# Performance work log

Hardware: AMD Instinct MI355X
Metric: run time of the kernel (lower is better)

## Reference

```python
import jax, jax.numpy as jnp
import numpy as np

B, D, E, K, H, C = 8192, 1024, 8, 2, 2048, 512
LN_EPS = 1e-5


def setup_inputs() -> dict:
    key = jax.random.key(0)
    ks = jax.random.split(key, 6)
    s = 0.02
    return {
        "x": jax.random.normal(ks[0], (B, D), dtype=jnp.float32),
        "Wr": jax.random.normal(ks[1], (E, D), dtype=jnp.float32) * s,  # router weight [E,D]
        "br": jnp.zeros((E,), dtype=jnp.float32),
        "gamma": jnp.ones((E, D), dtype=jnp.float32),   # per-expert LayerNorm scale
        "beta": jnp.zeros((E, D), dtype=jnp.float32),   # per-expert LayerNorm shift
        "W1": jax.random.normal(ks[2], (E, H, D), dtype=jnp.float32) * s,
        "b1": jnp.zeros((E, H), dtype=jnp.float32),
        "W2": jax.random.normal(ks[3], (E, C, H), dtype=jnp.float32) * s,
        "b2": jnp.zeros((E, C), dtype=jnp.float32),
    }


def reference(x, Wr, br, gamma, beta, W1, b1, W2, b2):
    # Router + top-k gating (softmax over the k selected logits only)
    router_logits = x @ Wr.T + br                       # [B,E]
    topk_vals, topk_idx = jax.lax.top_k(router_logits, K)  # [B,K]
    topk_w = jax.nn.softmax(topk_vals, axis=-1)         # [B,K]
    # Dense gate [B,E]: gate[b,e] = sum_j topk_w[b,j] * (topk_idx[b,j]==e)
    gate = (jax.nn.one_hot(topk_idx, E, dtype=x.dtype) * topk_w[..., None]).sum(axis=1)

    # LayerNorm statistics are expert-independent; affine is per-expert
    mu = x.mean(axis=-1, keepdims=True)
    var = ((x - mu) ** 2).mean(axis=-1, keepdims=True)
    xn = (x - mu) * jax.lax.rsqrt(var + LN_EPS)          # [B,D]

    out = jnp.zeros((x.shape[0], C), dtype=x.dtype)
    for e in range(E):  # small fixed expert count
        xe = xn * gamma[e] + beta[e]                     # [B,D]
        h = jax.nn.gelu(xe @ W1[e].T + b1[e], approximate=False)  # [B,H]
        y = h @ W2[e].T + b2[e]                          # [B,C]
        out = out + gate[:, e:e + 1] * y
    return out
```

## Files before the change

kernel.cpp:

```cpp
#include <hip/hip_runtime.h>
#include <hip/hip_bf16.h>
#include <math.h>

#define B_TOK 8192
#define DDIM 1024
#define NEXP 8
#define HDIM 2048
#define CDIM 512
#define LN_EPS 1e-5f
#define MAXT256 72
#define MAXROWS (MAXT256 * 256)

typedef __attribute__((ext_vector_type(4))) float f32x4;
typedef __attribute__((ext_vector_type(8))) short bf16x8;

__device__ __forceinline__ unsigned short f2bf(float f) {
  __hip_bfloat16 h = __float2bfloat16(f);
  return *reinterpret_cast<unsigned short*>(&h);
}
__device__ __forceinline__ float bf2f(unsigned short u) {
  unsigned int x = ((unsigned int)u) << 16;
  return *reinterpret_cast<float*>(&x);
}

__device__ __forceinline__ void gload_lds16(const unsigned short* g, unsigned short* l) {
  __builtin_amdgcn_global_load_lds(
      (const __attribute__((address_space(1))) unsigned int*)g,
      (__attribute__((address_space(3))) unsigned int*)l, 16, 0, 0);
}

__global__ __launch_bounds__(256) void router_ln_kernel(
    const float* __restrict__ x, const float* __restrict__ Wr,
    const float* __restrict__ br, int* __restrict__ eidx,
    float* __restrict__ wgt, unsigned short* __restrict__ xn) {
  const int wid = threadIdx.x >> 6;
  const int lane = threadIdx.x & 63;
  const int tok = blockIdx.x * 4 + wid;

  const float4* xr = reinterpret_cast<const float4*>(x + (size_t)tok * DDIM);
  float4 xv[4];
  float sum = 0.f, sumsq = 0.f;
  float dot[NEXP];
#pragma unroll
  for (int e = 0; e < NEXP; ++e) dot[e] = 0.f;

#pragma unroll
  for (int i = 0; i < 4; ++i) {
    const int f = i * 64 + lane;
    float4 v = xr[f];
    xv[i] = v;
    sum += v.x + v.y + v.z + v.w;
    sumsq += v.x * v.x + v.y * v.y + v.z * v.z + v.w * v.w;
#pragma unroll
    for (int e = 0; e < NEXP; ++e) {
      float4 w = reinterpret_cast<const float4*>(Wr + e * DDIM)[f];
      dot[e] += v.x * w.x + v.y * w.y + v.z * w.z + v.w * w.w;
    }
  }
#pragma unroll
  for (int off = 32; off > 0; off >>= 1) {
    sum += __shfl_xor(sum, off);
    sumsq += __shfl_xor(sumsq, off);
#pragma unroll
    for (int e = 0; e < NEXP; ++e) dot[e] += __shfl_xor(dot[e], off);
  }
  const float mu = sum * (1.f / DDIM);
  const float var = sumsq * (1.f / DDIM) - mu * mu;
  const float rs = rsqrtf(var + LN_EPS);

  float lg[NEXP];
#pragma unroll
  for (int e = 0; e < NEXP; ++e) lg[e] = dot[e] + br[e];

  int i1 = 0; float v1 = lg[0];
#pragma unroll
  for (int e = 1; e < NEXP; ++e) { if (lg[e] > v1) { v1 = lg[e]; i1 = e; } }
  int i2 = -1; float v2 = -3.4e38f;
#pragma unroll
  for (int e = 0; e < NEXP; ++e) { if (e != i1 && lg[e] > v2) { v2 = lg[e]; i2 = e; } }

  const float e2 = __expf(v2 - v1);
  const float inv = 1.f / (1.f + e2);
  if (lane == 0) {
    eidx[tok * 2] = i1; eidx[tok * 2 + 1] = i2;
    wgt[tok * 2] = inv; wgt[tok * 2 + 1] = e2 * inv;
  }

  unsigned short* xnr = xn + (size_t)tok * DDIM;
#pragma unroll
  for (int i = 0; i < 4; ++i) {
    const int f = i * 64 + lane;
    float4 v = xv[i];
    ushort4 o;
    o.x = f2bf((v.x - mu) * rs);
    o.y = f2bf((v.y - mu) * rs);
    o.z = f2bf((v.z - mu) * rs);
    o.w = f2bf((v.w - mu) * rs);
    reinterpret_cast<ushort4*>(xnr)[f] = o;
  }
}

__global__ __launch_bounds__(256) void sort_kernel(
    const int* __restrict__ eidx,
    int* __restrict__ tokRow,
    int* __restrict__ slot2row,
    int* __restrict__ tileExp,
    int* __restrict__ nTilesOut) {
  __shared__ int cnt[NEXP], segBase[NEXP], cur[NEXP];
  const int tid = threadIdx.x;
  if (tid < NEXP) { cnt[tid] = 0; cur[tid] = 0; }
  __syncthreads();
  for (int t = tid; t < B_TOK * 2; t += 256)
    atomicAdd(&cnt[eidx[t]], 1);
  __syncthreads();
  if (tid == 0) {
    int c = 0;
    for (int e = 0; e < NEXP; ++e) {
      segBase[e] = c;
      const int nt = (cnt[e] + 255) >> 8;
      for (int t = 0; t < nt; ++t) tileExp[(c >> 8) + t] = e;
      for (int p = c + cnt[e]; p < c + nt * 256; ++p) tokRow[p] = 0;
      c += nt * 256;
    }
    *nTilesOut = c >> 8;
  }
  __syncthreads();
  for (int t = tid; t < B_TOK * 2; t += 256) {
    const int e = eidx[t];
    const int pos = segBase[e] + atomicAdd(&cur[e], 1);
    tokRow[pos] = t >> 1;
    slot2row[t] = pos;
  }
}

__global__ __launch_bounds__(256) void prep_w1_kernel(
    const float* __restrict__ W1, const float* __restrict__ gamma,
    const float* __restrict__ beta, const float* __restrict__ b1,
    unsigned short* __restrict__ W1g, float* __restrict__ c1) {
  const int eh = blockIdx.x;
  const int e = eh >> 11;
  const int tid = threadIdx.x;

  float4 w = reinterpret_cast<const float4*>(W1 + (size_t)eh * DDIM)[tid];
  float4 g = reinterpret_cast<const float4*>(gamma + (size_t)e * DDIM)[tid];
  float4 bt = reinterpret_cast<const float4*>(beta + (size_t)e * DDIM)[tid];

  ushort4 o;
  o.x = f2bf(w.x * g.x); o.y = f2bf(w.y * g.y);
  o.z = f2bf(w.z * g.z); o.w = f2bf(w.w * g.w);
  reinterpret_cast<ushort4*>(W1g + (size_t)eh * DDIM)[tid] = o;

  float p = w.x * bt.x + w.y * bt.y + w.z * bt.z + w.w * bt.w;
#pragma unroll
  for (int off = 32; off > 0; off >>= 1) p += __shfl_xor(p, off);
  __shared__ float red[4];
  const int lane = tid & 63, wv = tid >> 6;
  if (lane == 0) red[wv] = p;
  __syncthreads();
  if (tid == 0) c1[eh] = b1[eh] + red[0] + red[1] + red[2] + red[3];
}

__global__ __launch_bounds__(256) void prep_w2_kernel(
    const float* __restrict__ W2, unsigned short* __restrict__ W2b) {
  const int idx = blockIdx.x * 256 + threadIdx.x;
  float4 w = reinterpret_cast<const float4*>(W2)[idx];
  ushort4 o;
  o.x = f2bf(w.x); o.y = f2bf(w.y); o.z = f2bf(w.z); o.w = f2bf(w.w);
  reinterpret_cast<ushort4*>(W2b)[idx] = o;
}

#define BM 128
#define BN 128
#define BKK 64

__global__ __launch_bounds__(256) void gemm1_gelu_kernel(
    const unsigned short* __restrict__ A,
    const unsigned short* __restrict__ W1g,
    const float* __restrict__ c1,
    const int* __restrict__ tokRow, const int* __restrict__ tileExp,
    const int* __restrict__ nTiles,
    unsigned short* __restrict__ Hout) {
  const int flat = blockIdx.x;
  const int p = flat & 7;
  const int q = flat >> 3;
  const int by = p * 2 + (q / 144);
  const int bx = q % 144;
  if ((bx >> 1) >= *nTiles) return;
  const int e = tileExp[bx >> 1];

  __shared__ unsigned short lA[BM * BKK];
  __shared__ unsigned short lB[BN * BKK];
  const int tid = threadIdx.x;
  const int lane = tid & 63;
  const int wid = tid >> 6;
  const int wr = wid >> 1, wc = wid & 1;
  const int l15 = lane & 15, l4 = lane >> 4;

  const unsigned short* Bbase = W1g + ((size_t)e * HDIM + (size_t)by * BN) * DDIM;

  const int r = tid >> 3;
  const int swz = ((tid & 7) ^ (r & 7)) * 8;
  const int dst = (tid & 7) * 8;
  int aRow[4];
#pragma unroll
  for (int i = 0; i < 4; ++i) aRow[i] = tokRow[bx * BM + i * 32 + r];

  f32x4 acc[4][4];
#pragma unroll
  for (int m = 0; m < 4; ++m)
#pragma unroll
    for (int n = 0; n < 4; ++n)
#pragma unroll
      for (int j = 0; j < 4; ++j) acc[m][n][j] = 0.f;

  for (int k0 = 0; k0 < DDIM; k0 += BKK) {
#pragma unroll
    for (int i = 0; i < 4; ++i)
      gload_lds16(A + (size_t)aRow[i] * DDIM + k0 + swz,
                  &lA[(i * 32 + r) * BKK + dst]);
#pragma unroll
    for (int i = 0; i < 4; ++i)
      gload_lds16(Bbase + (size_t)(i * 32 + r) * DDIM + k0 + swz,
                  &lB[(i * 32 + r) * BKK + dst]);
    __syncthreads();
#pragma unroll
    for (int kk = 0; kk < 2; ++kk) {
      bf16x8 af[4], bfr[4];
      const int slot = (((kk * 4 + l4) ^ (l15 & 7)) * 8);
#pragma unroll
      for (int m = 0; m < 4; ++m)
        af[m] = *reinterpret_cast<const bf16x8*>(
            &lA[(wr * 64 + m * 16 + l15) * BKK + slot]);
#pragma unroll
      for (int n = 0; n < 4; ++n)
        bfr[n] = *reinterpret_cast<const bf16x8*>(
            &lB[(wc * 64 + n * 16 + l15) * BKK + slot]);
#pragma unroll
      for (int m = 0; m < 4; ++m)
#pragma unroll
        for (int n = 0; n < 4; ++n)
          acc[m][n] = __builtin_amdgcn_mfma_f32_16x16x32_bf16(af[m], bfr[n], acc[m][n], 0, 0, 0);
    }
    __syncthreads();
  }

  const int row0 = bx * BM + wr * 64;
  const int col0 = by * BN + wc * 64;
  const float* bias = c1 + e * HDIM;
#pragma unroll
  for (int n = 0; n < 4; ++n) {
    const int col = col0 + n * 16 + l15;
    const float bv = bias[col];
#pragma unroll
    for (int m = 0; m < 4; ++m) {
#pragma unroll
      for (int j = 0; j < 4; ++j) {
        const int row = row0 + m * 16 + l4 * 4 + j;
        const float v = acc[m][n][j] + bv;
        const float gl = 0.5f * v * (1.f + erff(v * 0.70710678118654752f));
        Hout[(size_t)row * HDIM + col] = f2bf(gl);
      }
    }
  }
}

__global__ __launch_bounds__(256) void gemm2_kernel(
    const unsigned short* __restrict__ Hbuf,
    const unsigned short* __restrict__ W2b,
    const int* __restrict__ tileExp, const int* __restrict__ nTiles,
    unsigned short* __restrict__ Y) {
  const int flat = blockIdx.x;
  const int p = flat & 7;
  const int q = flat >> 3;
  const int by = p >> 1;
  const int bx = (p & 1) * 72 + q;
  if ((bx >> 1) >= *nTiles) return;
  const int e = tileExp[bx >> 1];

  __shared__ unsigned short lA[BM * BKK];
  __shared__ unsigned short lB[BN * BKK];
  const int tid = threadIdx.x;
  const int lane = tid & 63;
  const int wid = tid >> 6;
  const int wr = wid >> 1, wc = wid & 1;
  const int l15 = lane & 15, l4 = lane >> 4;

  const unsigned short* Abase = Hbuf + (size_t)bx * BM * HDIM;
  const unsigned short* Bbase = W2b + ((size_t)e * CDIM + (size_t)by * BN) * HDIM;

  f32x4 acc[4][4];
#pragma unroll
  for (int m = 0; m < 4; ++m)
#pragma unroll
    for (int n = 0; n < 4; ++n)
#pragma unroll
      for (int j = 0; j < 4; ++j) acc[m][n][j] = 0.f;

  const int r = tid >> 3;
  const int swz = ((tid & 7) ^ (r & 7)) * 8;
  const int dst = (tid & 7) * 8;

  for (int k0 = 0; k0 < HDIM; k0 += BKK) {
#pragma unroll
    for (int i = 0; i < 4; ++i)
      gload_lds16(Abase + (size_t)(i * 32 + r) * HDIM + k0 + swz,
                  &lA[(i * 32 + r) * BKK + dst]);
#pragma unroll
    for (int i = 0; i < 4; ++i)
      gload_lds16(Bbase + (size_t)(i * 32 + r) * HDIM + k0 + swz,
                  &lB[(i * 32 + r) * BKK + dst]);
    __syncthreads();
#pragma unroll
    for (int kk = 0; kk < 2; ++kk) {
      bf16x8 af[4], bfr[4];
      const int slot = (((kk * 4 + l4) ^ (l15 & 7)) * 8);
#pragma unroll
      for (int m = 0; m < 4; ++m)
        af[m] = *reinterpret_cast<const bf16x8*>(
            &lA[(wr * 64 + m * 16 + l15) * BKK + slot]);
#pragma unroll
      for (int n = 0; n < 4; ++n)
        bfr[n] = *reinterpret_cast<const bf16x8*>(
            &lB[(wc * 64 + n * 16 + l15) * BKK + slot]);
#pragma unroll
      for (int m = 0; m < 4; ++m)
#pragma unroll
        for (int n = 0; n < 4; ++n)
          acc[m][n] = __builtin_amdgcn_mfma_f32_16x16x32_bf16(af[m], bfr[n], acc[m][n], 0, 0, 0);
    }
    __syncthreads();
  }

  const int row0 = bx * BM + wr * 64;
  const int col0 = by * BN + wc * 64;
#pragma unroll
  for (int m = 0; m < 4; ++m) {
#pragma unroll
    for (int j = 0; j < 4; ++j) {
      const int row = row0 + m * 16 + l4 * 4 + j;
#pragma unroll
      for (int n = 0; n < 4; ++n) {
        const int col = col0 + n * 16 + l15;
        Y[(size_t)row * CDIM + col] = f2bf(acc[m][n][j]);
      }
    }
  }
}

__global__ __launch_bounds__(256) void combine_kernel(
    const unsigned short* __restrict__ Y, const int* __restrict__ slot2row,
    const int* __restrict__ eidx, const float* __restrict__ wgt,
    const float* __restrict__ b2, float* __restrict__ out) {
  const int idx = blockIdx.x * 256 + threadIdx.x;
  const int b = idx >> 7;
  const int c4 = (idx & 127) * 4;
  const int r0 = slot2row[b * 2], r1 = slot2row[b * 2 + 1];
  const int e0 = eidx[b * 2], e1 = eidx[b * 2 + 1];
  const float w0 = wgt[b * 2], w1 = wgt[b * 2 + 1];
  ushort4 y0 = *reinterpret_cast<const ushort4*>(Y + (size_t)r0 * CDIM + c4);
  ushort4 y1 = *reinterpret_cast<const ushort4*>(Y + (size_t)r1 * CDIM + c4);
  float4 bb0 = *reinterpret_cast<const float4*>(b2 + e0 * CDIM + c4);
  float4 bb1 = *reinterpret_cast<const float4*>(b2 + e1 * CDIM + c4);
  float4 o;
  o.x = w0 * (bf2f(y0.x) + bb0.x) + w1 * (bf2f(y1.x) + bb1.x);
  o.y = w0 * (bf2f(y0.y) + bb0.y) + w1 * (bf2f(y1.y) + bb1.y);
  o.z = w0 * (bf2f(y0.z) + bb0.z) + w1 * (bf2f(y1.z) + bb1.z);
  o.w = w0 * (bf2f(y0.w) + bb0.w) + w1 * (bf2f(y1.w) + bb1.w);
  *reinterpret_cast<float4*>(out + (size_t)b * CDIM + c4) = o;
}

extern "C" void kernel_launch(void* const* d_in, const int* in_sizes, int n_in,
                              void* d_out, int out_size, void* d_ws, size_t ws_size,
                              hipStream_t stream) {
  const float* x     = (const float*)d_in[0];
  const float* Wr    = (const float*)d_in[1];
  const float* br    = (const float*)d_in[2];
  const float* gamma = (const float*)d_in[3];
  const float* beta  = (const float*)d_in[4];
  const float* W1    = (const float*)d_in[5];
  const float* b1    = (const float*)d_in[6];
  const float* W2    = (const float*)d_in[7];
  const float* b2    = (const float*)d_in[8];
  float* out = (float*)d_out;

  char* ws = (char*)d_ws;
  unsigned short* xn   = (unsigned short*)(ws);
  unsigned short* W2b  = (unsigned short*)(ws);
  unsigned short* hbuf = (unsigned short*)(ws + (size_t)16 * 1048576);
  unsigned short* W1g  = (unsigned short*)(ws + (size_t)88 * 1048576);
  unsigned short* ybuf = (unsigned short*)(ws + (size_t)88 * 1048576);
  char* misc           = ws + (size_t)120 * 1048576;
  float* c1      = (float*)(misc);
  int* eidx      = (int*)(misc + 65536);
  float* wgt     = (float*)(misc + 2 * 65536);
  int* slot2row  = (int*)(misc + 3 * 65536);
  int* tokRow    = (int*)(misc + 4 * 65536);
  int* tileExp   = (int*)(misc + 4 * 65536 + 131072);
  int* nTiles    = tileExp + MAXT256;

  router_ln_kernel<<<dim3(B_TOK / 4), dim3(256), 0, stream>>>(x, Wr, br, eidx, wgt, xn);
  sort_kernel<<<dim3(1), dim3(256), 0, stream>>>(eidx, tokRow, slot2row, tileExp, nTiles);
  prep_w1_kernel<<<dim3(NEXP * HDIM), dim3(256), 0, stream>>>(W1, gamma, beta, b1, W1g, c1);

  gemm1_gelu_kernel<<<dim3(2304), dim3(256), 0, stream>>>(
      xn, W1g, c1, tokRow, tileExp, nTiles, hbuf);

  prep_w2_kernel<<<dim3((NEXP * CDIM * HDIM / 4) / 256), dim3(256), 0, stream>>>(W2, W2b);

  gemm2_kernel<<<dim3(576), dim3(256), 0, stream>>>(
      hbuf, W2b, tileExp, nTiles, ybuf);
  combine_kernel<<<dim3(B_TOK * CDIM / 4 / 256), dim3(256), 0, stream>>>(
      ybuf, slot2row, eidx, wgt, b2, out);
}
```

Baseline: 296.5 us.

## Swap MFMA operands for vector stores, tanh-GELU, smaller GEMM2 tiles, simpler block mapping

Both GEMMs now pass weights as the first MFMA operand, so each lane holds four consecutive output columns and can write them as one packed ushort4 with a float4 bias load. The exact erf GELU is replaced by a sigmoid-form tanh approximation built from exp and a fast reciprocal. GEMM2 uses a 128x64 tile and launches twice as many blocks to fill more CUs. The XCD-aware block remapping is dropped in favour of a plain flat mapping. The GELU approximation changes numerics slightly, and the new mapping may lose L2 locality.

```diff
diff --git a/kernel.cpp b/kernel.cpp
--- a/kernel.cpp
+++ b/kernel.cpp
@@ -21,6 +21,12 @@
 __device__ __forceinline__ float bf2f(unsigned short u) {
   unsigned int x = ((unsigned int)u) << 16;
   return *reinterpret_cast<float*>(&x);
+}
+
+__device__ __forceinline__ float gelu_f(float v) {
+  const float t = __builtin_fmaf(0.044715f * v, v, 1.0f);
+  const float u = -1.5957691216f * v * t;
+  return v * __builtin_amdgcn_rcpf(1.0f + __expf(u));
 }
 
 __device__ __forceinline__ void gload_lds16(const unsigned short* g, unsigned short* l) {
@@ -181,10 +187,8 @@
     const int* __restrict__ nTiles,
     unsigned short* __restrict__ Hout) {
   const int flat = blockIdx.x;
-  const int p = flat & 7;
-  const int q = flat >> 3;
-  const int by = p * 2 + (q / 144);
-  const int bx = q % 144;
+  const int by = flat & 15;
+  const int bx = flat >> 4;
   if ((bx >> 1) >= *nTiles) return;
   const int e = tileExp[bx >> 1];
 
@@ -207,11 +211,11 @@
 
   f32x4 acc[4][4];
 #pragma unroll
-  for (int m = 0; m < 4; ++m)
-#pragma unroll
-    for (int n = 0; n < 4; ++n)
-#pragma unroll
-      for (int j = 0; j < 4; ++j) acc[m][n][j] = 0.f;
+  for (int n = 0; n < 4; ++n)
+#pragma unroll
+    for (int m = 0; m < 4; ++m)
+#pragma unroll
+      for (int j = 0; j < 4; ++j) acc[n][m][j] = 0.f;
 
   for (int k0 = 0; k0 < DDIM; k0 += BKK) {
 #pragma unroll
@@ -225,44 +229,47 @@
     __syncthreads();
 #pragma unroll
     for (int kk = 0; kk < 2; ++kk) {
-      bf16x8 af[4], bfr[4];
+      bf16x8 xf[4], wf[4];
       const int slot = (((kk * 4 + l4) ^ (l15 & 7)) * 8);
 #pragma unroll
       for (int m = 0; m < 4; ++m)
-        af[m] = *reinterpret_cast<const bf16x8*>(
+        xf[m] = *reinterpret_cast<const bf16x8*>(
             &lA[(wr * 64 + m * 16 + l15) * BKK + slot]);
 #pragma unroll
       for (int n = 0; n < 4; ++n)
-        bfr[n] = *reinterpret_cast<const bf16x8*>(
+        wf[n] = *reinterpret_cast<const bf16x8*>(
             &lB[(wc * 64 + n * 16 + l15) * BKK + slot]);
 #pragma unroll
-      for (int m = 0; m < 4; ++m)
-#pragma unroll
-        for (int n = 0; n < 4; ++n)
-          acc[m][n] = __builtin_amdgcn_mfma_f32_16x16x32_bf16(af[m], bfr[n], acc[m][n], 0, 0, 0);
+      for (int n = 0; n < 4; ++n)
+#pragma unroll
+        for (int m = 0; m < 4; ++m)
+          acc[n][m] = __builtin_amdgcn_mfma_f32_16x16x32_bf16(wf[n], xf[m], acc[n][m], 0, 0, 0);
     }
     __syncthreads();
   }
 
   const int row0 = bx * BM + wr * 64;
   const int col0 = by * BN + wc * 64;
-  const float* bias = c1 + e * HDIM;
+  const float* biasp = c1 + e * HDIM;
 #pragma unroll
   for (int n = 0; n < 4; ++n) {
-    const int col = col0 + n * 16 + l15;
-    const float bv = bias[col];
+    const int hb = col0 + n * 16 + l4 * 4;
+    const float4 b4 = *reinterpret_cast<const float4*>(biasp + hb);
 #pragma unroll
     for (int m = 0; m < 4; ++m) {
-#pragma unroll
-      for (int j = 0; j < 4; ++j) {
-        const int row = row0 + m * 16 + l4 * 4 + j;
-        const float v = acc[m][n][j] + bv;
-        const float gl = 0.5f * v * (1.f + erff(v * 0.70710678118654752f));
-        Hout[(size_t)row * HDIM + col] = f2bf(gl);
-      }
-    }
-  }
-}
+      const int tokr = row0 + m * 16 + l15;
+      ushort4 o;
+      o.x = f2bf(gelu_f(acc[n][m][0] + b4.x));
+      o.y = f2bf(gelu_f(acc[n][m][1] + b4.y));
+      o.z = f2bf(gelu_f(acc[n][m][2] + b4.z));
+      o.w = f2bf(gelu_f(acc[n][m][3] + b4.w));
+      *reinterpret_cast<ushort4*>(&Hout[(size_t)tokr * HDIM + hb]) = o;
+    }
+  }
+}
+
+#define BM2 128
+#define BN2 64
 
 __global__ __launch_bounds__(256) void gemm2_kernel(
     const unsigned short* __restrict__ Hbuf,
@@ -270,31 +277,29 @@
     const int* __restrict__ tileExp, const int* __restrict__ nTiles,
     unsigned short* __restrict__ Y) {
   const int flat = blockIdx.x;
-  const int p = flat & 7;
-  const int q = flat >> 3;
-  const int by = p >> 1;
-  const int bx = (p & 1) * 72 + q;
+  const int by = flat & 7;
+  const int bx = flat >> 3;
   if ((bx >> 1) >= *nTiles) return;
   const int e = tileExp[bx >> 1];
 
-  __shared__ unsigned short lA[BM * BKK];
-  __shared__ unsigned short lB[BN * BKK];
+  __shared__ unsigned short lA[BM2 * BKK];
+  __shared__ unsigned short lB[BN2 * BKK];
   const int tid = threadIdx.x;
   const int lane = tid & 63;
   const int wid = tid >> 6;
   const int wr = wid >> 1, wc = wid & 1;
   const int l15 = lane & 15, l4 = lane >> 4;
 
-  const unsigned short* Abase = Hbuf + (size_t)bx * BM * HDIM;
-  const unsigned short* Bbase = W2b + ((size_t)e * CDIM + (size_t)by * BN) * HDIM;
-
-  f32x4 acc[4][4];
-#pragma unroll
-  for (int m = 0; m < 4; ++m)
-#pragma unroll
-    for (int n = 0; n < 4; ++n)
-#pragma unroll
-      for (int j = 0; j < 4; ++j) acc[m][n][j] = 0.f;
+  const unsigned short* Abase = Hbuf + (size_t)bx * BM2 * HDIM;
+  const unsigned short* Bbase = W2b + ((size_t)e * CDIM + (size_t)by * BN2) * HDIM;
+
+  f32x4 acc[2][4];
+#pragma unroll
+  for (int n = 0; n < 2; ++n)
+#pragma unroll
+    for (int m = 0; m < 4; ++m)
+#pragma unroll
+      for (int j = 0; j < 4; ++j) acc[n][m][j] = 0.f;
 
   const int r = tid >> 3;
   const int swz = ((tid & 7) ^ (r & 7)) * 8;
@@ -306,43 +311,45 @@
       gload_lds16(Abase + (size_t)(i * 32 + r) * HDIM + k0 + swz,
                   &lA[(i * 32 + r) * BKK + dst]);
 #pragma unroll
-    for (int i = 0; i < 4; ++i)
+    for (int i = 0; i < 2; ++i)
       gload_lds16(Bbase + (size_t)(i * 32 + r) * HDIM + k0 + swz,
                   &lB[(i * 32 + r) * BKK + dst]);
     __syncthreads();
 #pragma unroll
     for (int kk = 0; kk < 2; ++kk) {
-      bf16x8 af[4], bfr[4];
+      bf16x8 xf[4], wf[2];
       const int slot = (((kk * 4 + l4) ^ (l15 & 7)) * 8);
 #pragma unroll
       for (int m = 0; m < 4; ++m)
-        af[m] = *reinterpret_cast<const bf16x8*>(
+        xf[m] = *reinterpret_cast<const bf16x8*>(
             &lA[(wr * 64 + m * 16 + l15) * BKK + slot]);
 #pragma unroll
-      for (int n = 0; n < 4; ++n)
-        bfr[n] = *reinterpret_cast<const bf16x8*>(
-            &lB[(wc * 64 + n * 16 + l15) * BKK + slot]);
-#pragma unroll
-      for (int m = 0; m < 4; ++m)
-#pragma unroll
-        for (int n = 0; n < 4; ++n)
-          acc[m][n] = __builtin_amdgcn_mfma_f32_16x16x32_bf16(af[m], bfr[n], acc[m][n], 0, 0, 0);
+      for (int n = 0; n < 2; ++n)
+        wf[n] = *reinterpret_cast<const bf16x8*>(
+            &lB[(wc * 32 + n * 16 + l15) * BKK + slot]);
+#pragma unroll
+      for (int n = 0; n < 2; ++n)
+#pragma unroll
+        for (int m = 0; m < 4; ++m)
+          acc[n][m] = __builtin_amdgcn_mfma_f32_16x16x32_bf16(wf[n], xf[m], acc[n][m], 0, 0, 0);
     }
     __syncthreads();
   }
 
-  const int row0 = bx * BM + wr * 64;
-  const int col0 = by * BN + wc * 64;
-#pragma unroll
-  for (int m = 0; m < 4; ++m) {
-#pragma unroll
-    for (int j = 0; j < 4; ++j) {
-      const int row = row0 + m * 16 + l4 * 4 + j;
-#pragma unroll
-      for (int n = 0; n < 4; ++n) {
-        const int col = col0 + n * 16 + l15;
-        Y[(size_t)row * CDIM + col] = f2bf(acc[m][n][j]);
-      }
+  const int row0 = bx * BM2 + wr * 64;
+  const int col0 = by * BN2 + wc * 32;
+#pragma unroll
+  for (int n = 0; n < 2; ++n) {
+    const int cb = col0 + n * 16 + l4 * 4;
+#pragma unroll
+    for (int m = 0; m < 4; ++m) {
+      const int tokr = row0 + m * 16 + l15;
+      ushort4 o;
+      o.x = f2bf(acc[n][m][0]);
+      o.y = f2bf(acc[n][m][1]);
+      o.z = f2bf(acc[n][m][2]);
+      o.w = f2bf(acc[n][m][3]);
+      *reinterpret_cast<ushort4*>(&Y[(size_t)tokr * CDIM + cb]) = o;
     }
   }
 }
@@ -407,7 +414,7 @@
 
   prep_w2_kernel<<<dim3((NEXP * CDIM * HDIM / 4) / 256), dim3(256), 0, stream>>>(W2, W2b);
 
-  gemm2_kernel<<<dim3(576), dim3(256), 0, stream>>>(
+  gemm2_kernel<<<dim3(1152), dim3(256), 0, stream>>>(
       hbuf, W2b, tileExp, nTiles, ybuf);
   combine_kernel<<<dim3(B_TOK * CDIM / 4 / 256), dim3(256), 0, stream>>>(
       ybuf, slot2row, eidx, wgt, b2, out);
```

Result: slower. 303.7 us (+2.5%).
